# Optimization experiments

Measured on AMD Instinct MI355X. Metric: run time of the kernel, lower is better.

Reference implementation:

```python
import jax, jax.numpy as jnp
import numpy as np

N_NODES = 163840
N_EDGES = 2621440
F_IN = 64
F_HID = 64
SUBG = 20  # size_subgraph_samples
NEG_SLOPE = 0.2


def gat_conv(x, src, dst, W, a_src, a_dst, b):
    """PyG GATConv, heads=1, concat. src/dst already include self-loops."""
    n = x.shape[0]
    h = x @ W                               # [N, H]
    al_s = h @ a_src                        # [N]
    al_d = h @ a_dst                        # [N]
    e = jax.nn.leaky_relu(al_s[src] + al_d[dst], NEG_SLOPE)  # [E]
    # softmax over incoming edges of each dst node
    m = jax.ops.segment_max(e, dst, num_segments=n)
    ex = jnp.exp(e - m[dst])
    denom = jax.ops.segment_sum(ex, dst, num_segments=n)
    alpha = ex / (denom[dst] + 1e-16)
    msg = h[src] * alpha[:, None]           # [E, H]
    out = jax.ops.segment_sum(msg, dst, num_segments=n)
    return out + b


def setup_inputs() -> dict:
    key = jax.random.key(0)
    ks = jax.random.split(key, 12)
    s = 0.05
    return {
        "x": jax.random.normal(ks[0], (N_NODES, F_IN), jnp.float32),
        "edge_index": jax.random.randint(ks[1], (2, N_EDGES), 0, N_NODES, jnp.int64 if jax.config.jax_enable_x64 else jnp.int32),
        "W1": jax.random.normal(ks[2], (F_IN, F_HID), jnp.float32) * s,
        "a_src1": jax.random.normal(ks[3], (F_HID,), jnp.float32) * s,
        "a_dst1": jax.random.normal(ks[4], (F_HID,), jnp.float32) * s,
        "b1": jnp.zeros((F_HID,), jnp.float32),
        "W2": jax.random.normal(ks[5], (F_HID, F_HID), jnp.float32) * s,
        "a_src2": jax.random.normal(ks[6], (F_HID,), jnp.float32) * s,
        "a_dst2": jax.random.normal(ks[7], (F_HID,), jnp.float32) * s,
        "b2": jnp.zeros((F_HID,), jnp.float32),
        "W_out": jax.random.normal(ks[8], (F_HID * SUBG, 1), jnp.float32) * s,
        "b_out": jnp.zeros((1,), jnp.float32),
    }


def reference(x, edge_index, W1, a_src1, a_dst1, b1, W2, a_src2, a_dst2, b2, W_out, b_out):
    n = x.shape[0]
    loop = jnp.arange(n, dtype=edge_index.dtype)
    src = jnp.concatenate([edge_index[0], loop])  # add_self_loops=True
    dst = jnp.concatenate([edge_index[1], loop])
    h = gat_conv(x, src, dst, W1, a_src1, a_dst1, b1)
    h = jax.nn.relu(h)  # dropout is identity in eval mode
    h = gat_conv(h, src, dst, W2, a_src2, a_dst2, b2)
    h = jax.nn.relu(h)
    h = h.reshape(n // SUBG, F_HID * SUBG)
    return h @ W_out + b_out
```

## Files before the change

kernel.cpp:

```cpp
#include <hip/hip_runtime.h>
#include <math.h>

#define F 64
#define NPB 160
#define STAGE_CAP 6304

typedef __attribute__((ext_vector_type(8))) short bf16x8;
typedef __attribute__((ext_vector_type(4))) float f32x4;

__device__ inline unsigned short f2bf(float f) {
  unsigned int u = __float_as_uint(f);
  u += 0x7fffu + ((u >> 16) & 1u);
  return (unsigned short)(u >> 16);
}


__global__ __launch_bounds__(256) void k_bin_count(const int* __restrict__ edst, int* __restrict__ cntT,
                                                   int e, int ch, int nblk, int nb) {
  __shared__ int h[1024];
  int k = blockIdx.x, tid = threadIdx.x;
  for (int i = tid; i < nb; i += 256) h[i] = 0;
  __syncthreads();
  int beg = k * ch, end = min(e, beg + ch);
  for (int i = beg + tid; i < end; i += 256) atomicAdd(&h[edst[i] / NPB], 1);
  __syncthreads();
  for (int b = tid; b < nb; b += 256) cntT[b * nblk + k] = h[b];
}

__global__ __launch_bounds__(256) void k_scan1(const int* __restrict__ counts, int* __restrict__ offs,
                                               int* __restrict__ bsums, int n) {
  int tid = threadIdx.x, lane = tid & 63, wv = tid >> 6;
  int i = blockIdx.x * 256 + tid;
  int v = (i < n) ? counts[i] : 0;
  int x = v;
  #pragma unroll
  for (int o = 1; o <= 32; o <<= 1) { int y = __shfl_up(x, o); if (lane >= o) x += y; }
  __shared__ int wsum[4];
  if (lane == 63) wsum[wv] = x;
  __syncthreads();
  int add = 0;
  for (int w = 0; w < wv; w++) add += wsum[w];
  int incl = x + add;
  if (i < n) offs[i] = incl - v;
  if (tid == 255) bsums[blockIdx.x] = incl;
}

__global__ __launch_bounds__(256) void k_scan2(int* __restrict__ bs, int nb) {
  __shared__ int wsum[4];
  __shared__ int carry_sh;
  int tid = threadIdx.x, lane = tid & 63, wv = tid >> 6;
  if (tid == 0) carry_sh = 0;
  __syncthreads();
  for (int base = 0; base < nb; base += 256) {
    int i = base + tid;
    int v = (i < nb) ? bs[i] : 0;
    int x = v;
    #pragma unroll
    for (int o = 1; o <= 32; o <<= 1) { int y = __shfl_up(x, o); if (lane >= o) x += y; }
    if (lane == 63) wsum[wv] = x;
    __syncthreads();
    int add = 0;
    for (int w = 0; w < wv; w++) add += wsum[w];
    int incl = x + add;
    int carry = carry_sh;
    if (i < nb) bs[i] = incl - v + carry;
    __syncthreads();
    if (tid == 255) carry_sh = carry + incl;
    __syncthreads();
  }
}

__global__ __launch_bounds__(256) void k_bin_scatter(const int* __restrict__ esrc, const int* __restrict__ edst,
                                                     const int* __restrict__ posT, const int* __restrict__ bsums,
                                                     unsigned int* __restrict__ binned,
                                                     int e, int ch, int nblk, int nb) {
  __shared__ int cur[1024];
  int k = blockIdx.x, tid = threadIdx.x;
  for (int b = tid; b < nb; b += 256) {
    int idx = b * nblk + k;
    cur[b] = posT[idx] + bsums[idx >> 8];
  }
  __syncthreads();
  int beg = k * ch, end = min(e, beg + ch);
  for (int i = beg + tid; i < end; i += 256) {
    int d = edst[i];
    int b = d / NPB;
    unsigned int ld = (unsigned int)(d - b * NPB);
    int p = atomicAdd(&cur[b], 1);
    binned[p] = (unsigned int)esrc[i] | (ld << 24);
  }
}

__global__ __launch_bounds__(256) void k_bucket_csr(const unsigned int* __restrict__ binned,
                                                    const int* __restrict__ posT, const int* __restrict__ bsums,
                                                    int* __restrict__ ssrc, int* __restrict__ offs,
                                                    int n, int nblk, int nb, int e) {
  __shared__ int ncnt[NPB];
  __shared__ int noff[NPB];
  __shared__ int cur[NPB];
  __shared__ int sc[256];
  __shared__ int stage[STAGE_CAP];
  int b = blockIdx.x, tid = threadIdx.x;
  int node0 = b * NPB;
  int nn = min(NPB, n - node0);
  int i0 = b * nblk;
  int ebeg = posT[i0] + bsums[i0 >> 8];
  int eend;
  if (b == nb - 1) eend = e;
  else { int i1 = (b + 1) * nblk; eend = posT[i1] + bsums[i1 >> 8]; }
  int ecnt = eend - ebeg;
  for (int i = tid; i < NPB; i += 256) ncnt[i] = 0;
  __syncthreads();
  for (int i = tid; i < ecnt; i += 256) { unsigned int v = binned[ebeg + i]; atomicAdd(&ncnt[v >> 24], 1); }
  __syncthreads();
  int x = (tid < nn) ? ncnt[tid] + 1 : 0;
  sc[tid] = x;
  __syncthreads();
  #pragma unroll
  for (int o = 1; o < 256; o <<= 1) {
    int y = (tid >= o) ? sc[tid - o] : 0;
    __syncthreads();
    sc[tid] += y;
    __syncthreads();
  }
  if (tid < nn) noff[tid] = sc[tid] - x;
  __syncthreads();
  int tot = ecnt + nn;
  int outbase = ebeg + node0;
  bool staged = (tot <= STAGE_CAP);
  if (tid < nn) {
    cur[tid] = noff[tid] + 1;
    offs[node0 + tid] = outbase + noff[tid];
    if (staged) stage[noff[tid]] = node0 + tid;
    else        ssrc[outbase + noff[tid]] = node0 + tid;
  }
  __syncthreads();
  if (staged) {
    for (int i = tid; i < ecnt; i += 256) {
      unsigned int v = binned[ebeg + i];
      int p = atomicAdd(&cur[v >> 24], 1);
      stage[p] = (int)(v & 0xFFFFFFu);
    }
    __syncthreads();
    for (int i = tid; i < tot; i += 256) ssrc[outbase + i] = stage[i];
  } else {
    for (int i = tid; i < ecnt; i += 256) {
      unsigned int v = binned[ebeg + i];
      int p = atomicAdd(&cur[v >> 24], 1);
      ssrc[outbase + p] = (int)(v & 0xFFFFFFu);
    }
  }
  if (b == 0 && tid == 0) offs[n] = e + n;
}

template<bool IN_BF16>
__global__ __launch_bounds__(256) void k_gemm(const void* __restrict__ in, const float* __restrict__ W,
                                              const float* __restrict__ avs, const float* __restrict__ avd,
                                              unsigned short* __restrict__ hgb, float* __restrict__ als,
                                              float* __restrict__ ald, int n) {
  int tid = threadIdx.x, lane = tid & 63, wv = tid >> 6;
  int l15 = lane & 15, quad = lane >> 4;
  bf16x8 bfr[4][2];
  #pragma unroll
  for (int c = 0; c < 4; c++) {
    #pragma unroll
    for (int kk = 0; kk < 2; kk++) {
      #pragma unroll
      for (int j = 0; j < 8; j++) {
        int k = kk * 32 + quad * 8 + j;
        bfr[c][kk][j] = (short)f2bf(W[k * F + c * 16 + l15]);
      }
    }
  }
  float as_l[4], ad_l[4];
  #pragma unroll
  for (int c = 0; c < 4; c++) { as_l[c] = avs[c * 16 + l15]; ad_l[c] = avd[c * 16 + l15]; }

  int nchunks = n >> 6;
  for (int chunk = blockIdx.x; chunk < nchunks; chunk += gridDim.x) {
    int r0 = (chunk << 6) + (wv << 4);
    bf16x8 a0, a1;
    if constexpr (IN_BF16) {
      const uint4* row4 = (const uint4*)((const unsigned short*)in + (size_t)(r0 + l15) * F);
      uint4 u0 = row4[quad];
      uint4 u1 = row4[quad + 4];
      a0 = *(const bf16x8*)&u0;
      a1 = *(const bf16x8*)&u1;
    } else {
      const float4* xr = (const float4*)((const float*)in + (size_t)(r0 + l15) * F + quad * 8);
      float4 xa = xr[0], xb = xr[1];
      float4 xc = xr[8], xd = xr[9];
      a0[0] = (short)f2bf(xa.x); a0[1] = (short)f2bf(xa.y); a0[2] = (short)f2bf(xa.z); a0[3] = (short)f2bf(xa.w);
      a0[4] = (short)f2bf(xb.x); a0[5] = (short)f2bf(xb.y); a0[6] = (short)f2bf(xb.z); a0[7] = (short)f2bf(xb.w);
      a1[0] = (short)f2bf(xc.x); a1[1] = (short)f2bf(xc.y); a1[2] = (short)f2bf(xc.z); a1[3] = (short)f2bf(xc.w);
      a1[4] = (short)f2bf(xd.x); a1[5] = (short)f2bf(xd.y); a1[6] = (short)f2bf(xd.z); a1[7] = (short)f2bf(xd.w);
    }
    f32x4 cfr[4];
    #pragma unroll
    for (int c = 0; c < 4; c++) {
      cfr[c] = (f32x4){0.f, 0.f, 0.f, 0.f};
      cfr[c] = __builtin_amdgcn_mfma_f32_16x16x32_bf16(a0, bfr[c][0], cfr[c], 0, 0, 0);
      cfr[c] = __builtin_amdgcn_mfma_f32_16x16x32_bf16(a1, bfr[c][1], cfr[c], 0, 0, 0);
    }
    #pragma unroll
    for (int i = 0; i < 4; i++) {
      int row = r0 + quad * 4 + i;
      #pragma unroll
      for (int c = 0; c < 4; c++) hgb[(size_t)row * F + c * 16 + l15] = f2bf(cfr[c][i]);
      float ps = cfr[0][i] * as_l[0] + cfr[1][i] * as_l[1] + cfr[2][i] * as_l[2] + cfr[3][i] * as_l[3];
      float pd = cfr[0][i] * ad_l[0] + cfr[1][i] * ad_l[1] + cfr[2][i] * ad_l[2] + cfr[3][i] * ad_l[3];
      #pragma unroll
      for (int o = 1; o <= 8; o <<= 1) { ps += __shfl_xor(ps, o); pd += __shfl_xor(pd, o); }
      if (l15 == 0) { als[row] = ps; ald[row] = pd; }
    }
  }
}

template<bool OUT_BF16>
__global__ __launch_bounds__(256) void k_spmm(const int* __restrict__ offs, const int* __restrict__ ssrc,
                                              const unsigned short* __restrict__ hgb,
                                              const float* __restrict__ als, const float* __restrict__ ald,
                                              const float* __restrict__ bias, void* __restrict__ outp, int n) {
  int tid = threadIdx.x, lane = tid & 63, wv = tid >> 6;
  int g8 = lane >> 3, l8 = lane & 7;
  const uint4* hg4 = (const uint4*)hgb;
  float4 bl0 = ((const float4*)bias)[l8 * 2];
  float4 bl1 = ((const float4*)bias)[l8 * 2 + 1];

  int node = (blockIdx.x * 4 + wv) * 8 + g8;
  int cnode = min(node, n - 1);
  bool nodeok = node < n;
  int beg = offs[cnode];
  int deg = nodeok ? (offs[cnode + 1] - beg) : 0;
  int degc = max(deg - 1, 0);
  float aldv = ald[cnode];

  int dm = deg;
  #pragma unroll
  for (int o = 8; o <= 32; o <<= 1) dm = max(dm, __shfl_xor(dm, o));

  float s = 0.f;
  float acc[8];
  #pragma unroll
  for (int k = 0; k < 8; k++) acc[k] = 0.f;

  #pragma unroll 2
  for (int j = 0; j < dm; j++) {
    int jj = min(j, degc);
    int src = ssrc[beg + jj];
    float t = als[src] + aldv;
    t = fmaxf(t, 0.2f * t);
    float ex = (j < deg) ? __expf(t) : 0.f;
    s += ex;
    uint4 u = hg4[(size_t)src * 8 + l8];
    acc[0] = fmaf(ex, __uint_as_float(u.x << 16), acc[0]);
    acc[1] = fmaf(ex, __uint_as_float(u.x & 0xffff0000u), acc[1]);
    acc[2] = fmaf(ex, __uint_as_float(u.y << 16), acc[2]);
    acc[3] = fmaf(ex, __uint_as_float(u.y & 0xffff0000u), acc[3]);
    acc[4] = fmaf(ex, __uint_as_float(u.z << 16), acc[4]);
    acc[5] = fmaf(ex, __uint_as_float(u.z & 0xffff0000u), acc[5]);
    acc[6] = fmaf(ex, __uint_as_float(u.w << 16), acc[6]);
    acc[7] = fmaf(ex, __uint_as_float(u.w & 0xffff0000u), acc[7]);
  }

  if (nodeok) {
    float iv = 1.f / (s + 1e-16f);
    float r[8];
    r[0] = fmaxf(fmaf(acc[0], iv, bl0.x), 0.f);
    r[1] = fmaxf(fmaf(acc[1], iv, bl0.y), 0.f);
    r[2] = fmaxf(fmaf(acc[2], iv, bl0.z), 0.f);
    r[3] = fmaxf(fmaf(acc[3], iv, bl0.w), 0.f);
    r[4] = fmaxf(fmaf(acc[4], iv, bl1.x), 0.f);
    r[5] = fmaxf(fmaf(acc[5], iv, bl1.y), 0.f);
    r[6] = fmaxf(fmaf(acc[6], iv, bl1.z), 0.f);
    r[7] = fmaxf(fmaf(acc[7], iv, bl1.w), 0.f);
    if constexpr (OUT_BF16) {
      unsigned short p[8];
      #pragma unroll
      for (int k = 0; k < 8; k++) p[k] = f2bf(r[k]);
      ((uint4*)outp)[(size_t)node * 8 + l8] = *(const uint4*)p;
    } else {
      float4* o4 = (float4*)outp + (size_t)node * 16 + l8 * 2;
      o4[0] = make_float4(r[0], r[1], r[2], r[3]);
      o4[1] = make_float4(r[4], r[5], r[6], r[7]);
    }
  }
}

__global__ __launch_bounds__(256) void k_final(const float* __restrict__ h, const float* __restrict__ Wout,
                                               const float* __restrict__ bout, float* __restrict__ out,
                                               int ng) {
  int tid = threadIdx.x, lane = tid & 63, wv = tid >> 6;
  int g = blockIdx.x * 4 + wv;
  if (g >= ng) return;
  const float4* h4 = (const float4*)h + (size_t)g * 320;
  const float4* w4 = (const float4*)Wout;
  float sacc = 0.f;
  #pragma unroll
  for (int k = 0; k < 5; k++) {
    float4 a = h4[k * 64 + lane];
    float4 b = w4[k * 64 + lane];
    sacc += a.x * b.x + a.y * b.y + a.z * b.z + a.w * b.w;
  }
  #pragma unroll
  for (int o = 32; o >= 1; o >>= 1) sacc += __shfl_xor(sacc, o);
  if (lane == 0) out[g] = sacc + bout[0];
}

extern "C" void kernel_launch(void* const* d_in, const int* in_sizes, int n_in,
                              void* d_out, int out_size, void* d_ws, size_t ws_size,
                              hipStream_t stream) {
  const float* x   = (const float*)d_in[0];
  const int*   ei  = (const int*)d_in[1];
  const float* W1  = (const float*)d_in[2];
  const float* as1 = (const float*)d_in[3];
  const float* ad1 = (const float*)d_in[4];
  const float* b1  = (const float*)d_in[5];
  const float* W2  = (const float*)d_in[6];
  const float* as2 = (const float*)d_in[7];
  const float* ad2 = (const float*)d_in[8];
  const float* b2  = (const float*)d_in[9];
  const float* Wo  = (const float*)d_in[10];
  const float* bo  = (const float*)d_in[11];
  float* out = (float*)d_out;

  const int N = in_sizes[0] / F;
  const int E = in_sizes[1] / 2;
  const int* esrc = ei;
  const int* edst = ei + E;

  size_t off = 0;
  auto alloc = [&](size_t bytes) -> void* {
    void* p = (char*)d_ws + off;
    off += (bytes + 255) & ~(size_t)255;
    return p;
  };
  float* A    = (float*)alloc((size_t)N * F * 4);
  unsigned short* hgb = (unsigned short*)alloc((size_t)N * F * 2);
  float* als  = (float*)alloc((size_t)N * 4);
  float* ald  = (float*)alloc((size_t)N * 4);
  int* offs   = (int*)alloc((size_t)(N + 1) * 4);
  int* bsums  = (int*)alloc(8192);
  int* ssrc   = (int*)alloc((size_t)(E + N) * 4);
  (void)ws_size; (void)n_in; (void)out_size;

  const int NBLK = 256;
  const int NB = (N + NPB - 1) / NPB;
  const int CH = (E + NBLK - 1) / NBLK;
  const int FLAT = NB * NBLK;

  int* cntT = (int*)A;
  int* posT = (int*)((char*)A + ((size_t)FLAT * 4 + 1024));
  unsigned int* binned = (unsigned int*)hgb;

  int gF = (FLAT + 255) / 256;

  k_bin_count<<<NBLK, 256, 0, stream>>>(edst, cntT, E, CH, NBLK, NB);
  k_scan1<<<gF, 256, 0, stream>>>(cntT, posT, bsums, FLAT);
  k_scan2<<<1, 256, 0, stream>>>(bsums, gF);
  k_bin_scatter<<<NBLK, 256, 0, stream>>>(esrc, edst, posT, bsums, binned, E, CH, NBLK, NB);
  k_bucket_csr<<<NB, 256, 0, stream>>>(binned, posT, bsums, ssrc, offs, N, NBLK, NB, E);

  int gSp = (N + 31) / 32;
  k_gemm<false><<<2560, 256, 0, stream>>>(x, W1, as1, ad1, hgb, als, ald, N);
  k_spmm<true><<<gSp, 256, 0, stream>>>(offs, ssrc, hgb, als, ald, b1, A, N);
  k_gemm<true><<<2560, 256, 0, stream>>>(A, W2, as2, ad2, hgb, als, ald, N);
  k_spmm<false><<<gSp, 256, 0, stream>>>(offs, ssrc, hgb, als, ald, b2, A, N);
  int NG = N / 20;
  k_final<<<(NG + 3) / 4, 256, 0, stream>>>(A, Wo, bo, out, NG);
}
```

Baseline: 318.3 us.

## Sort nodes by degree for SpMM balance and fuse final linear into layer-2 aggregation

Adds a degree histogram and counting-sort pass that orders nodes by descending in-degree, so each wavefront's 8 nodes have similar degrees and the padded loop to the max degree wastes fewer iterations. The second-layer SpMM now computes the dot with W_out in registers and atomically accumulates into the per-group output, removing the float hidden write and the separate final kernel. The cost is three extra small kernels, scattered node order that hurts output/ald locality, and float atomics whose summation order is nondeterministic.

```diff
diff --git a/kernel.cpp b/kernel.cpp
--- a/kernel.cpp
+++ b/kernel.cpp
@@ -45,10 +45,11 @@
   if (tid == 255) bsums[blockIdx.x] = incl;
 }
 
-__global__ __launch_bounds__(256) void k_scan2(int* __restrict__ bs, int nb) {
+__global__ __launch_bounds__(256) void k_scan2(int* __restrict__ bs, int nb, int* __restrict__ dh) {
   __shared__ int wsum[4];
   __shared__ int carry_sh;
   int tid = threadIdx.x, lane = tid & 63, wv = tid >> 6;
+  if (tid < 64) dh[tid] = 0;
   if (tid == 0) carry_sh = 0;
   __syncthreads();
   for (int base = 0; base < nb; base += 256) {
@@ -153,6 +154,41 @@
   if (b == 0 && tid == 0) offs[n] = e + n;
 }
 
+
+__global__ __launch_bounds__(256) void k_deghist(const int* __restrict__ offs, int* __restrict__ dh, int n) {
+  __shared__ int h[64];
+  int tid = threadIdx.x;
+  if (tid < 64) h[tid] = 0;
+  __syncthreads();
+  int i = blockIdx.x * 256 + tid;
+  if (i < n) { int d = offs[i + 1] - offs[i]; atomicAdd(&h[min(d, 63)], 1); }
+  __syncthreads();
+  if (tid < 64 && h[tid]) atomicAdd(&dh[tid], h[tid]);
+}
+
+__global__ void k_degbase(const int* __restrict__ dh, int* __restrict__ cursor) {
+  if (threadIdx.x == 0) {
+    int acc = 0;
+    for (int b = 63; b >= 0; b--) { cursor[b] = acc; acc += dh[b]; }
+  }
+}
+
+__global__ __launch_bounds__(256) void k_degscatter(const int* __restrict__ offs, int* __restrict__ cursor,
+                                                    int* __restrict__ order, int n) {
+  __shared__ int h[64];
+  __shared__ int base[64];
+  int tid = threadIdx.x;
+  if (tid < 64) h[tid] = 0;
+  __syncthreads();
+  int i = blockIdx.x * 256 + tid;
+  int bin = 0, rank = 0;
+  if (i < n) { int d = offs[i + 1] - offs[i]; bin = min(d, 63); rank = atomicAdd(&h[bin], 1); }
+  __syncthreads();
+  if (tid < 64 && h[tid]) base[tid] = atomicAdd(&cursor[tid], h[tid]);
+  __syncthreads();
+  if (i < n) order[base[bin] + rank] = i;
+}
+
 template<bool IN_BF16>
 __global__ __launch_bounds__(256) void k_gemm(const void* __restrict__ in, const float* __restrict__ W,
                                               const float* __restrict__ avs, const float* __restrict__ avd,
@@ -216,24 +252,27 @@
   }
 }
 
-template<bool OUT_BF16>
+template<int MODE>
 __global__ __launch_bounds__(256) void k_spmm(const int* __restrict__ offs, const int* __restrict__ ssrc,
+                                              const int* __restrict__ order,
                                               const unsigned short* __restrict__ hgb,
                                               const float* __restrict__ als, const float* __restrict__ ald,
-                                              const float* __restrict__ bias, void* __restrict__ outp, int n) {
+                                              const float* __restrict__ bias, const float* __restrict__ Wout,
+                                              void* __restrict__ outp, int n) {
   int tid = threadIdx.x, lane = tid & 63, wv = tid >> 6;
   int g8 = lane >> 3, l8 = lane & 7;
   const uint4* hg4 = (const uint4*)hgb;
   float4 bl0 = ((const float4*)bias)[l8 * 2];
   float4 bl1 = ((const float4*)bias)[l8 * 2 + 1];
 
-  int node = (blockIdx.x * 4 + wv) * 8 + g8;
-  int cnode = min(node, n - 1);
-  bool nodeok = node < n;
-  int beg = offs[cnode];
-  int deg = nodeok ? (offs[cnode + 1] - beg) : 0;
+  int idx = (blockIdx.x * 4 + wv) * 8 + g8;
+  int cidx = min(idx, n - 1);
+  bool nodeok = idx < n;
+  int node = order[cidx];
+  int beg = offs[node];
+  int deg = nodeok ? (offs[node + 1] - beg) : 0;
   int degc = max(deg - 1, 0);
-  float aldv = ald[cnode];
+  float aldv = ald[node];
 
   int dm = deg;
   #pragma unroll
@@ -263,48 +302,37 @@
     acc[7] = fmaf(ex, __uint_as_float(u.w & 0xffff0000u), acc[7]);
   }
 
-  if (nodeok) {
-    float iv = 1.f / (s + 1e-16f);
-    float r[8];
-    r[0] = fmaxf(fmaf(acc[0], iv, bl0.x), 0.f);
-    r[1] = fmaxf(fmaf(acc[1], iv, bl0.y), 0.f);
-    r[2] = fmaxf(fmaf(acc[2], iv, bl0.z), 0.f);
-    r[3] = fmaxf(fmaf(acc[3], iv, bl0.w), 0.f);
-    r[4] = fmaxf(fmaf(acc[4], iv, bl1.x), 0.f);
-    r[5] = fmaxf(fmaf(acc[5], iv, bl1.y), 0.f);
-    r[6] = fmaxf(fmaf(acc[6], iv, bl1.z), 0.f);
-    r[7] = fmaxf(fmaf(acc[7], iv, bl1.w), 0.f);
-    if constexpr (OUT_BF16) {
-      unsigned short p[8];
-      #pragma unroll
-      for (int k = 0; k < 8; k++) p[k] = f2bf(r[k]);
-      ((uint4*)outp)[(size_t)node * 8 + l8] = *(const uint4*)p;
-    } else {
-      float4* o4 = (float4*)outp + (size_t)node * 16 + l8 * 2;
-      o4[0] = make_float4(r[0], r[1], r[2], r[3]);
-      o4[1] = make_float4(r[4], r[5], r[6], r[7]);
-    }
-  }
-}
-
-__global__ __launch_bounds__(256) void k_final(const float* __restrict__ h, const float* __restrict__ Wout,
-                                               const float* __restrict__ bout, float* __restrict__ out,
-                                               int ng) {
-  int tid = threadIdx.x, lane = tid & 63, wv = tid >> 6;
-  int g = blockIdx.x * 4 + wv;
-  if (g >= ng) return;
-  const float4* h4 = (const float4*)h + (size_t)g * 320;
-  const float4* w4 = (const float4*)Wout;
-  float sacc = 0.f;
-  #pragma unroll
-  for (int k = 0; k < 5; k++) {
-    float4 a = h4[k * 64 + lane];
-    float4 b = w4[k * 64 + lane];
-    sacc += a.x * b.x + a.y * b.y + a.z * b.z + a.w * b.w;
-  }
-  #pragma unroll
-  for (int o = 32; o >= 1; o >>= 1) sacc += __shfl_xor(sacc, o);
-  if (lane == 0) out[g] = sacc + bout[0];
+  if (!nodeok) return;
+  float iv = 1.f / (s + 1e-16f);
+  float r[8];
+  r[0] = fmaxf(fmaf(acc[0], iv, bl0.x), 0.f);
+  r[1] = fmaxf(fmaf(acc[1], iv, bl0.y), 0.f);
+  r[2] = fmaxf(fmaf(acc[2], iv, bl0.z), 0.f);
+  r[3] = fmaxf(fmaf(acc[3], iv, bl0.w), 0.f);
+  r[4] = fmaxf(fmaf(acc[4], iv, bl1.x), 0.f);
+  r[5] = fmaxf(fmaf(acc[5], iv, bl1.y), 0.f);
+  r[6] = fmaxf(fmaf(acc[6], iv, bl1.z), 0.f);
+  r[7] = fmaxf(fmaf(acc[7], iv, bl1.w), 0.f);
+  if constexpr (MODE == 0) {
+    unsigned short p[8];
+    #pragma unroll
+    for (int k = 0; k < 8; k++) p[k] = f2bf(r[k]);
+    ((uint4*)outp)[(size_t)node * 8 + l8] = *(const uint4*)p;
+  } else {
+    int grp = node / 20, slot = node - grp * 20;
+    const float* wr = Wout + slot * F + l8 * 8;
+    float dot = 0.f;
+    #pragma unroll
+    for (int k = 0; k < 8; k++) dot = fmaf(r[k], wr[k], dot);
+    #pragma unroll
+    for (int o = 1; o <= 4; o <<= 1) dot += __shfl_xor(dot, o);
+    if (l8 == 0) atomicAdd((float*)outp + grp, dot);
+  }
+}
+
+__global__ __launch_bounds__(256) void k_outinit(float* __restrict__ out, const float* __restrict__ bo, int ng) {
+  int i = blockIdx.x * 256 + threadIdx.x;
+  if (i < ng) out[i] = bo[0];
 }
 
 extern "C" void kernel_launch(void* const* d_in, const int* in_sizes, int n_in,
@@ -342,6 +370,9 @@
   int* offs   = (int*)alloc((size_t)(N + 1) * 4);
   int* bsums  = (int*)alloc(8192);
   int* ssrc   = (int*)alloc((size_t)(E + N) * 4);
+  int* order  = (int*)alloc((size_t)N * 4);
+  int* dh     = (int*)alloc(256);
+  int* dcur   = (int*)alloc(256);
   (void)ws_size; (void)n_in; (void)out_size;
 
   const int NBLK = 256;
@@ -354,18 +385,23 @@
   unsigned int* binned = (unsigned int*)hgb;
 
   int gF = (FLAT + 255) / 256;
+  int gN = (N + 255) / 256;
 
   k_bin_count<<<NBLK, 256, 0, stream>>>(edst, cntT, E, CH, NBLK, NB);
   k_scan1<<<gF, 256, 0, stream>>>(cntT, posT, bsums, FLAT);
-  k_scan2<<<1, 256, 0, stream>>>(bsums, gF);
+  k_scan2<<<1, 256, 0, stream>>>(bsums, gF, dh);
   k_bin_scatter<<<NBLK, 256, 0, stream>>>(esrc, edst, posT, bsums, binned, E, CH, NBLK, NB);
   k_bucket_csr<<<NB, 256, 0, stream>>>(binned, posT, bsums, ssrc, offs, N, NBLK, NB, E);
 
+  k_deghist<<<gN, 256, 0, stream>>>(offs, dh, N);
+  k_degbase<<<1, 64, 0, stream>>>(dh, dcur);
+  k_degscatter<<<gN, 256, 0, stream>>>(offs, dcur, order, N);
+
   int gSp = (N + 31) / 32;
   k_gemm<false><<<2560, 256, 0, stream>>>(x, W1, as1, ad1, hgb, als, ald, N);
-  k_spmm<true><<<gSp, 256, 0, stream>>>(offs, ssrc, hgb, als, ald, b1, A, N);
+  k_spmm<0><<<gSp, 256, 0, stream>>>(offs, ssrc, order, hgb, als, ald, b1, nullptr, A, N);
   k_gemm<true><<<2560, 256, 0, stream>>>(A, W2, as2, ad2, hgb, als, ald, N);
-  k_spmm<false><<<gSp, 256, 0, stream>>>(offs, ssrc, hgb, als, ald, b2, A, N);
   int NG = N / 20;
-  k_final<<<(NG + 3) / 4, 256, 0, stream>>>(A, Wo, bo, out, NG);
-}
+  k_outinit<<<(NG + 255) / 256, 256, 0, stream>>>(out, bo, NG);
+  k_spmm<1><<<gSp, 256, 0, stream>>>(offs, ssrc, order, hgb, als, ald, b2, Wo, out, N);
+}
```

Result: slower. 332.4 us (+4.4%).

## Fuse final linear into second SpMM and prepack bf16 weights once

Applied to the files above, without the earlier changes.

Drops the k_final kernel. The second SpMM now dots each node's ReLU output with its slot of W_out and atomically adds the result into the per-group output, which k_scan2 pre-initialises with the bias. Weight conversion to bf16 MFMA fragments moves into an extra block of k_bin_count, so the GEMM blocks load prepacked uint4 fragments instead of each converting W. This removes the fp32 hidden write and read plus one launch, at the cost of float atomics that make summation order nondeterministic.

```diff
diff --git a/kernel.cpp b/kernel.cpp
--- a/kernel.cpp
+++ b/kernel.cpp
@@ -16,9 +16,28 @@
 
 
 __global__ __launch_bounds__(256) void k_bin_count(const int* __restrict__ edst, int* __restrict__ cntT,
-                                                   int e, int ch, int nblk, int nb) {
+                                                   int e, int ch, int nblk, int nb,
+                                                   const float* __restrict__ W1, const float* __restrict__ W2,
+                                                   uint4* __restrict__ wf) {
   __shared__ int h[1024];
   int k = blockIdx.x, tid = threadIdx.x;
+  if (k == nblk) {
+    for (int i = tid; i < 1024; i += 256) {
+      int layer = i >> 9, rem = i & 511;
+      int cb = rem >> 6, lane = rem & 63;
+      int c = cb >> 1, kk = cb & 1;
+      int l15 = lane & 15, quad = lane >> 4;
+      const float* W = layer ? W2 : W1;
+      unsigned short p[8];
+      #pragma unroll
+      for (int j = 0; j < 8; j++) {
+        int kd = kk * 32 + quad * 8 + j;
+        p[j] = f2bf(W[kd * F + c * 16 + l15]);
+      }
+      wf[i] = *(const uint4*)p;
+    }
+    return;
+  }
   for (int i = tid; i < nb; i += 256) h[i] = 0;
   __syncthreads();
   int beg = k * ch, end = min(e, beg + ch);
@@ -45,10 +64,13 @@
   if (tid == 255) bsums[blockIdx.x] = incl;
 }
 
-__global__ __launch_bounds__(256) void k_scan2(int* __restrict__ bs, int nb) {
+__global__ __launch_bounds__(256) void k_scan2(int* __restrict__ bs, int nb,
+                                               float* __restrict__ out, const float* __restrict__ bo, int ng) {
   __shared__ int wsum[4];
   __shared__ int carry_sh;
   int tid = threadIdx.x, lane = tid & 63, wv = tid >> 6;
+  float b0 = bo[0];
+  for (int i = tid; i < ng; i += 256) out[i] = b0;
   if (tid == 0) carry_sh = 0;
   __syncthreads();
   for (int base = 0; base < nb; base += 256) {
@@ -154,7 +176,7 @@
 }
 
 template<bool IN_BF16>
-__global__ __launch_bounds__(256) void k_gemm(const void* __restrict__ in, const float* __restrict__ W,
+__global__ __launch_bounds__(256) void k_gemm(const void* __restrict__ in, const uint4* __restrict__ wf,
                                               const float* __restrict__ avs, const float* __restrict__ avd,
                                               unsigned short* __restrict__ hgb, float* __restrict__ als,
                                               float* __restrict__ ald, int n) {
@@ -162,15 +184,9 @@
   int l15 = lane & 15, quad = lane >> 4;
   bf16x8 bfr[4][2];
   #pragma unroll
-  for (int c = 0; c < 4; c++) {
-    #pragma unroll
-    for (int kk = 0; kk < 2; kk++) {
-      #pragma unroll
-      for (int j = 0; j < 8; j++) {
-        int k = kk * 32 + quad * 8 + j;
-        bfr[c][kk][j] = (short)f2bf(W[k * F + c * 16 + l15]);
-      }
-    }
+  for (int cb = 0; cb < 8; cb++) {
+    uint4 u = wf[cb * 64 + lane];
+    bfr[cb >> 1][cb & 1] = *(const bf16x8*)&u;
   }
   float as_l[4], ad_l[4];
   #pragma unroll
@@ -216,11 +232,12 @@
   }
 }
 
-template<bool OUT_BF16>
+template<int MODE>
 __global__ __launch_bounds__(256) void k_spmm(const int* __restrict__ offs, const int* __restrict__ ssrc,
                                               const unsigned short* __restrict__ hgb,
                                               const float* __restrict__ als, const float* __restrict__ ald,
-                                              const float* __restrict__ bias, void* __restrict__ outp, int n) {
+                                              const float* __restrict__ bias, const float* __restrict__ Wout,
+                                              void* __restrict__ outp, int n) {
   int tid = threadIdx.x, lane = tid & 63, wv = tid >> 6;
   int g8 = lane >> 3, l8 = lane & 7;
   const uint4* hg4 = (const uint4*)hgb;
@@ -263,48 +280,32 @@
     acc[7] = fmaf(ex, __uint_as_float(u.w & 0xffff0000u), acc[7]);
   }
 
-  if (nodeok) {
-    float iv = 1.f / (s + 1e-16f);
-    float r[8];
-    r[0] = fmaxf(fmaf(acc[0], iv, bl0.x), 0.f);
-    r[1] = fmaxf(fmaf(acc[1], iv, bl0.y), 0.f);
-    r[2] = fmaxf(fmaf(acc[2], iv, bl0.z), 0.f);
-    r[3] = fmaxf(fmaf(acc[3], iv, bl0.w), 0.f);
-    r[4] = fmaxf(fmaf(acc[4], iv, bl1.x), 0.f);
-    r[5] = fmaxf(fmaf(acc[5], iv, bl1.y), 0.f);
-    r[6] = fmaxf(fmaf(acc[6], iv, bl1.z), 0.f);
-    r[7] = fmaxf(fmaf(acc[7], iv, bl1.w), 0.f);
-    if constexpr (OUT_BF16) {
-      unsigned short p[8];
-      #pragma unroll
-      for (int k = 0; k < 8; k++) p[k] = f2bf(r[k]);
-      ((uint4*)outp)[(size_t)node * 8 + l8] = *(const uint4*)p;
-    } else {
-      float4* o4 = (float4*)outp + (size_t)node * 16 + l8 * 2;
-      o4[0] = make_float4(r[0], r[1], r[2], r[3]);
-      o4[1] = make_float4(r[4], r[5], r[6], r[7]);
-    }
-  }
-}
-
-__global__ __launch_bounds__(256) void k_final(const float* __restrict__ h, const float* __restrict__ Wout,
-                                               const float* __restrict__ bout, float* __restrict__ out,
-                                               int ng) {
-  int tid = threadIdx.x, lane = tid & 63, wv = tid >> 6;
-  int g = blockIdx.x * 4 + wv;
-  if (g >= ng) return;
-  const float4* h4 = (const float4*)h + (size_t)g * 320;
-  const float4* w4 = (const float4*)Wout;
-  float sacc = 0.f;
-  #pragma unroll
-  for (int k = 0; k < 5; k++) {
-    float4 a = h4[k * 64 + lane];
-    float4 b = w4[k * 64 + lane];
-    sacc += a.x * b.x + a.y * b.y + a.z * b.z + a.w * b.w;
-  }
-  #pragma unroll
-  for (int o = 32; o >= 1; o >>= 1) sacc += __shfl_xor(sacc, o);
-  if (lane == 0) out[g] = sacc + bout[0];
+  if (!nodeok) return;
+  float iv = 1.f / (s + 1e-16f);
+  float r[8];
+  r[0] = fmaxf(fmaf(acc[0], iv, bl0.x), 0.f);
+  r[1] = fmaxf(fmaf(acc[1], iv, bl0.y), 0.f);
+  r[2] = fmaxf(fmaf(acc[2], iv, bl0.z), 0.f);
+  r[3] = fmaxf(fmaf(acc[3], iv, bl0.w), 0.f);
+  r[4] = fmaxf(fmaf(acc[4], iv, bl1.x), 0.f);
+  r[5] = fmaxf(fmaf(acc[5], iv, bl1.y), 0.f);
+  r[6] = fmaxf(fmaf(acc[6], iv, bl1.z), 0.f);
+  r[7] = fmaxf(fmaf(acc[7], iv, bl1.w), 0.f);
+  if constexpr (MODE == 0) {
+    unsigned short p[8];
+    #pragma unroll
+    for (int k = 0; k < 8; k++) p[k] = f2bf(r[k]);
+    ((uint4*)outp)[(size_t)node * 8 + l8] = *(const uint4*)p;
+  } else {
+    int grp = node / 20, slot = node - grp * 20;
+    const float* wr = Wout + slot * F + l8 * 8;
+    float dot = 0.f;
+    #pragma unroll
+    for (int k = 0; k < 8; k++) dot = fmaf(r[k], wr[k], dot);
+    #pragma unroll
+    for (int o = 1; o <= 4; o <<= 1) dot += __shfl_xor(dot, o);
+    if (l8 == 0) atomicAdd((float*)outp + grp, dot);
+  }
 }
 
 extern "C" void kernel_launch(void* const* d_in, const int* in_sizes, int n_in,
@@ -342,6 +343,7 @@
   int* offs   = (int*)alloc((size_t)(N + 1) * 4);
   int* bsums  = (int*)alloc(8192);
   int* ssrc   = (int*)alloc((size_t)(E + N) * 4);
+  uint4* wf   = (uint4*)alloc(16384);
   (void)ws_size; (void)n_in; (void)out_size;
 
   const int NBLK = 256;
@@ -354,18 +356,17 @@
   unsigned int* binned = (unsigned int*)hgb;
 
   int gF = (FLAT + 255) / 256;
-
-  k_bin_count<<<NBLK, 256, 0, stream>>>(edst, cntT, E, CH, NBLK, NB);
+  int NG = N / 20;
+
+  k_bin_count<<<NBLK + 1, 256, 0, stream>>>(edst, cntT, E, CH, NBLK, NB, W1, W2, wf);
   k_scan1<<<gF, 256, 0, stream>>>(cntT, posT, bsums, FLAT);
-  k_scan2<<<1, 256, 0, stream>>>(bsums, gF);
+  k_scan2<<<1, 256, 0, stream>>>(bsums, gF, out, bo, NG);
   k_bin_scatter<<<NBLK, 256, 0, stream>>>(esrc, edst, posT, bsums, binned, E, CH, NBLK, NB);
   k_bucket_csr<<<NB, 256, 0, stream>>>(binned, posT, bsums, ssrc, offs, N, NBLK, NB, E);
 
   int gSp = (N + 31) / 32;
-  k_gemm<false><<<2560, 256, 0, stream>>>(x, W1, as1, ad1, hgb, als, ald, N);
-  k_spmm<true><<<gSp, 256, 0, stream>>>(offs, ssrc, hgb, als, ald, b1, A, N);
-  k_gemm<true><<<2560, 256, 0, stream>>>(A, W2, as2, ad2, hgb, als, ald, N);
-  k_spmm<false><<<gSp, 256, 0, stream>>>(offs, ssrc, hgb, als, ald, b2, A, N);
-  int NG = N / 20;
-  k_final<<<(NG + 3) / 4, 256, 0, stream>>>(A, Wo, bo, out, NG);
-}
+  k_gemm<false><<<2560, 256, 0, stream>>>(x, wf, as1, ad1, hgb, als, ald, N);
+  k_spmm<0><<<gSp, 256, 0, stream>>>(offs, ssrc, hgb, als, ald, b1, nullptr, A, N);
+  k_gemm<true><<<2560, 256, 0, stream>>>(A, wf + 512, as2, ad2, hgb, als, ald, N);
+  k_spmm<1><<<gSp, 256, 0, stream>>>(offs, ssrc, hgb, als, ald, b2, Wo, out, N);
+}
```

New measurement: 319.6 us. Within noise of the previous version (+0.4%).
